# Optimization experiments

Hardware: AMD Instinct MI355X
Metric: run time of the kernel (lower is better)

The kernel has to match this reference:

```python
import jax, jax.numpy as jnp
import numpy as np

STRIDES = (4, 8, 16, 32, 64)
RATIOS = (0.5, 1.0, 2.0)
SCALE = 8.0
A = 3
PRE_NMS = 2000
MAX_PER_IMG = 1000
NMS_THR = 0.7
MAX_RATIO = float(abs(np.log(16.0 / 1000.0)))  # wh_ratio_clip = 16/1000
LEVEL_OFFSET = 4096.0  # > max image coordinate, separates levels for batched NMS
FEAT_HW = ((208, 336), (104, 168), (52, 84), (26, 42), (13, 21))
N = 8


def grid_anchors(stride, H, W):
    # mmdet-style base anchors: scale 8, ratios (0.5,1,2), centered at 0
    r = jnp.asarray(RATIOS, jnp.float32)
    h_r = jnp.sqrt(r)
    w_r = 1.0 / h_r
    ws = stride * w_r * SCALE
    hs = stride * h_r * SCALE
    base = jnp.stack([-ws / 2, -hs / 2, ws / 2, hs / 2], axis=-1)  # [A,4]
    sx = jnp.arange(W, dtype=jnp.float32) * stride
    sy = jnp.arange(H, dtype=jnp.float32) * stride
    yy, xx = jnp.meshgrid(sy, sx, indexing='ij')
    shifts = jnp.stack([xx, yy, xx, yy], axis=-1).reshape(-1, 4)  # [H*W,4], row-major
    return (shifts[:, None, :] + base[None, :, :]).reshape(-1, 4)  # [H*W*A,4]


def decode(anchors, deltas, h, w):
    # DeltaXYWH decode with means 0, stds 1, clip to image
    px = (anchors[..., 0] + anchors[..., 2]) * 0.5
    py = (anchors[..., 1] + anchors[..., 3]) * 0.5
    pw = anchors[..., 2] - anchors[..., 0]
    ph = anchors[..., 3] - anchors[..., 1]
    dx, dy = deltas[..., 0], deltas[..., 1]
    dw = jnp.clip(deltas[..., 2], -MAX_RATIO, MAX_RATIO)
    dh = jnp.clip(deltas[..., 3], -MAX_RATIO, MAX_RATIO)
    gx = px + pw * dx
    gy = py + ph * dy
    gw = pw * jnp.exp(dw)
    gh = ph * jnp.exp(dh)
    x1 = jnp.clip(gx - gw * 0.5, 0.0, w)
    y1 = jnp.clip(gy - gh * 0.5, 0.0, h)
    x2 = jnp.clip(gx + gw * 0.5, 0.0, w)
    y2 = jnp.clip(gy + gh * 0.5, 0.0, h)
    return jnp.stack([x1, y1, x2, y2], axis=-1)


def iou_matrix(b):
    area = (b[:, 2] - b[:, 0]) * (b[:, 3] - b[:, 1])
    lt = jnp.maximum(b[:, None, :2], b[None, :, :2])
    rb = jnp.minimum(b[:, None, 2:], b[None, :, 2:])
    wh = jnp.clip(rb - lt, 0.0, None)
    inter = wh[..., 0] * wh[..., 1]
    union = area[:, None] + area[None, :] - inter
    return inter / jnp.maximum(union, 1e-6)


def _forward(cls_list, reg_list, image_h, image_w):
    scores_all, deltas_all, anchors_all, levels_all = [], [], [], []
    for lvl, (cls, reg) in enumerate(zip(cls_list, reg_list)):
        n, _, H, W = cls.shape
        anchors = grid_anchors(STRIDES[lvl], H, W)  # [H*W*A,4]
        s = jax.nn.sigmoid(jnp.transpose(cls, (0, 2, 3, 1)).reshape(n, -1))
        d = jnp.transpose(reg, (0, 2, 3, 1)).reshape(n, -1, 4)
        k = min(PRE_NMS, s.shape[1])  # topk pre-selection per level
        sv, si = jax.lax.top_k(s, k)
        dv = jnp.take_along_axis(d, si[..., None], axis=1)
        av = anchors[si]
        scores_all.append(sv)
        deltas_all.append(dv)
        anchors_all.append(av)
        levels_all.append(jnp.full((k,), lvl, jnp.int32))
    scores = jnp.concatenate(scores_all, axis=1)    # [N,M]
    deltas = jnp.concatenate(deltas_all, axis=1)    # [N,M,4]
    anchors = jnp.concatenate(anchors_all, axis=1)  # [N,M,4]
    levels = jnp.concatenate(levels_all)            # [M] (same per image)
    boxes = decode(anchors, deltas, float(image_h), float(image_w))
    # filter_boxes with min_area = prod((0,0)) = 0: keep boxes with area >= 0
    area = (boxes[..., 2] - boxes[..., 0]) * (boxes[..., 3] - boxes[..., 1])
    scores = jnp.where(area >= 0.0, scores, -1.0)
    M = boxes.shape[1]
    idxs = jnp.arange(M)

    def nms_one(bs):
        b_i, s_i = bs
        order = jnp.argsort(-s_i)
        b = b_i[order]
        s = s_i[order]
        lv = levels[order]
        # batched NMS: offset each level so cross-level boxes never overlap
        ob = jax.lax.stop_gradient(b + (lv.astype(b.dtype) * LEVEL_OFFSET)[:, None])
        iou = iou_matrix(ob)  # [M,M]

        def body(i, keep):
            sup = (iou[i] > NMS_THR) & (idxs > i) & keep[i]
            return keep & (~sup)

        keep = jax.lax.fori_loop(0, M, body, jnp.ones((M,), bool))
        rank = jnp.cumsum(keep.astype(jnp.int32)) - 1
        tgt = jnp.where(keep & (rank < MAX_PER_IMG), rank, MAX_PER_IMG)  # dump slot
        out_b = jnp.zeros((MAX_PER_IMG + 1, 4), b.dtype).at[tgt].set(b)[:MAX_PER_IMG]
        out_s = jnp.zeros((MAX_PER_IMG + 1,), s.dtype).at[tgt].set(s)[:MAX_PER_IMG]
        return out_b, out_s

    pb, ps = jax.lax.map(nms_one, (boxes, scores))  # sequential per image
    return pb, ps  # [N,1000,4], [N,1000] (zero-padded)


def setup_inputs() -> dict:
    key = jax.random.key(0)
    inp = {}
    for lvl, (H, W) in enumerate(FEAT_HW):
        k1 = jax.random.fold_in(key, 2 * lvl)
        k2 = jax.random.fold_in(key, 2 * lvl + 1)
        inp[f"class_out_{lvl}"] = jax.random.normal(k1, (N, A, H, W), jnp.float32)
        inp[f"reg_out_{lvl}"] = jax.random.normal(k2, (N, 4 * A, H, W), jnp.float32)
    inp["image_h"] = 832
    inp["image_w"] = 1344
    return inp


def reference(class_out_0, class_out_1, class_out_2, class_out_3, class_out_4,
              reg_out_0, reg_out_1, reg_out_2, reg_out_3, reg_out_4,
              image_h, image_w):
    cls_list = [class_out_0, class_out_1, class_out_2, class_out_3, class_out_4]
    reg_list = [reg_out_0, reg_out_1, reg_out_2, reg_out_3, reg_out_4]
    return _forward(cls_list, reg_list, image_h, image_w)
```

## Files before the change

kernel.cpp:

```cpp
#include <hip/hip_runtime.h>
#include <cmath>

#pragma clang fp contract(off)

namespace {
constexpr int NIMG = 8;
constexpr int NLVL = 5;
constexpr int LH[5]   = {208,104,52,26,13};
constexpr int LW[5]   = {336,168,84,42,21};
constexpr int LSTR[5] = {4,8,16,32,64};
constexpr int HWA[5]  = {209664,52416,13104,3276,819};
constexpr int KSEL[5] = {2000,2000,2000,2000,819};
constexpr int SOFF[5] = {0,2000,4000,6000,8000};
constexpr int MTOT    = 8819;
constexpr int CAP     = 6144;
constexpr int NPAIR   = NIMG*NLVL;
constexpr int CCUM[5] = {52,65,69,70,71};
constexpr int BLK_PER_IMG = 71;
constexpr int MASK_W  = 32;
constexpr int OUTK    = 1000;

constexpr size_t OFF_HIST   = 0;
constexpr size_t OFF_PKC    = 0;
constexpr size_t OFF_CNT    = 655360;
constexpr size_t OFF_THR    = 655520;
constexpr size_t ZERO_BYTES = 655680;
constexpr size_t OFF_CAND   = 655872;
constexpr size_t OFF_SELIDX = 1638912;
constexpr size_t OFF_SELKEY = 1921120;
constexpr size_t OFF_SELSC  = 2485536;
constexpr size_t OFF_SELBOX = 2767744;
constexpr size_t OFF_MASK   = 3896576;
constexpr size_t OFF_CKEY   = OFF_MASK;
constexpr size_t OFF_KEEP   = 24376576;
}

struct Ins {
  const float* cls[5];
  const float* reg[5];
  const int* ih;
  const int* iw;
};

__device__ __forceinline__ void decode_block(int b, int& img, int& lvl, int& chunk) {
  img = b / BLK_PER_IMG;
  int rb = b - img*BLK_PER_IMG;
  if      (rb < CCUM[0]) { lvl=0; chunk=rb; }
  else if (rb < CCUM[1]) { lvl=1; chunk=rb-CCUM[0]; }
  else if (rb < CCUM[2]) { lvl=2; chunk=rb-CCUM[1]; }
  else if (rb < CCUM[3]) { lvl=3; chunk=rb-CCUM[2]; }
  else                   { lvl=4; chunk=0; }
}

__device__ __forceinline__ unsigned mapbits(float x) {
  unsigned u = __float_as_uint(x);
  return u ^ (unsigned)(((int)u >> 31) | (int)0x80000000);
}

__device__ __forceinline__ float sigmoid_ref(float x) {
  float e = (float)exp(-(double)x);
  return 1.0f / (1.0f + e);
}

__global__ void k_hist(Ins in, unsigned* __restrict__ hist) {
  int img, lvl, chunk; decode_block(blockIdx.x, img, lvl, chunk);
  __shared__ unsigned lh[4096];
  for (int i = threadIdx.x; i < 4096; i += 256) lh[i] = 0;
  __syncthreads();
  const float* src = in.cls[lvl] + (size_t)img * HWA[lvl];
  int base = chunk * 4096;
  #pragma unroll
  for (int j = 0; j < 16; j++) {
    int e = base + j*256 + threadIdx.x;
    if (e < HWA[lvl]) {
      unsigned m = mapbits(src[e]);
      atomicAdd(&lh[m >> 20], 1u);
    }
  }
  __syncthreads();
  unsigned* gh = hist + (img*NLVL + lvl) * 4096;
  for (int i = threadIdx.x; i < 4096; i += 256)
    if (lh[i]) atomicAdd(&gh[i], lh[i]);
}

__global__ void k_scan(const unsigned* __restrict__ hist, unsigned* __restrict__ thr) {
  int pair = blockIdx.x; int lvl = pair % NLVL;
  const unsigned* h = hist + (size_t)pair * 4096;
  __shared__ unsigned part[256];
  unsigned s = 0;
  #pragma unroll
  for (int i = 0; i < 16; i++) s += h[threadIdx.x*16 + i];
  part[threadIdx.x] = s;
  __syncthreads();
  if (threadIdx.x == 0) {
    unsigned k = (unsigned)KSEL[lvl];
    unsigned cum = 0;
    unsigned edge = 0;
    for (int t = 255; t >= 0; t--) {
      if (cum + part[t] >= k) {
        for (int b = t*16 + 15; b >= t*16; b--) {
          cum += h[b];
          if (cum >= k) { edge = (unsigned)b; break; }
        }
        thr[pair] = edge << 20;
        return;
      }
      cum += part[t];
    }
    thr[pair] = 0u;
  }
}

__global__ void __launch_bounds__(256) k_compact(Ins in, const unsigned* __restrict__ thr,
                          unsigned* __restrict__ cnt, unsigned* __restrict__ cand,
                          unsigned long long* __restrict__ ckey) {
  int img, lvl, chunk; decode_block(blockIdx.x, img, lvl, chunk);
  int pair = img*NLVL + lvl;
  unsigned T = thr[pair];
  const float* src = in.cls[lvl] + (size_t)img * HWA[lvl];
  int hw = LH[lvl] * LW[lvl];
  int base = chunk * 4096;
  int lid = threadIdx.x & 63;
  __shared__ unsigned lbuf[4096];
  __shared__ unsigned long long lkey[4096];
  __shared__ unsigned lc, gbase;
  if (threadIdx.x == 0) lc = 0;
  __syncthreads();
  #pragma unroll
  for (int j = 0; j < 16; j++) {
    int e = base + j*256 + threadIdx.x;
    float v = 0.0f;
    bool inb = (e < HWA[lvl]);
    if (inb) v = src[e];
    bool sel = inb && (mapbits(v) >= T);
    unsigned long long mask = __ballot(sel);
    if (mask != 0ull) {
      int leader = __ffsll((long long)mask) - 1;
      unsigned wb = 0;
      if (lid == leader) wb = atomicAdd(&lc, (unsigned)__popcll(mask));
      wb = (unsigned)__shfl((int)wb, leader, 64);
      if (sel) {
        unsigned p = wb + (unsigned)__popcll(mask & ((1ull << lid) - 1ull));
        int a = e / hw;
        int r = e - a*hw;
        unsigned idx = (unsigned)(r*3 + a);
        lbuf[p] = idx;
        float s = sigmoid_ref(v);
        unsigned pack = ((unsigned)lvl << 18) | idx;
        lkey[p] = ((unsigned long long)__float_as_uint(s) << 21)
                | (unsigned long long)(0x1FFFFFu - pack);
      }
    }
  }
  __syncthreads();
  if (threadIdx.x == 0) gbase = atomicAdd(&cnt[pair], lc);
  __syncthreads();
  unsigned nsel = lc, gb = gbase;
  for (unsigned t = threadIdx.x; t < nsel; t += 256) {
    unsigned p = gb + t;
    if (p < CAP) {
      cand[(size_t)pair*CAP + p] = lbuf[t];
      ckey[(size_t)pair*CAP + p] = lkey[t];
    }
  }
}

__global__ void __launch_bounds__(256) k_rank(const unsigned* __restrict__ cntA,
                       const unsigned* __restrict__ cand,
                       const unsigned long long* __restrict__ ckey,
                       unsigned* __restrict__ sel_idx,
                       unsigned long long* __restrict__ sel_key,
                       float* __restrict__ sel_sc) {
  int pair = blockIdx.y; int tile = blockIdx.x;
  int img = pair / NLVL, lvl = pair % NLVL;
  int c = min((int)cntA[pair], CAP);
  if (tile*256 >= c) return;
  __shared__ unsigned long long keys[CAP];
  const unsigned long long* kp = ckey + (size_t)pair*CAP;
  for (int j = threadIdx.x; j < c; j += 256) keys[j] = kp[j];
  __syncthreads();
  int jj = tile*256 + threadIdx.x;
  if (jj >= c) return;
  unsigned long long mykey = keys[jj];
  int rk = 0;
  for (int j = 0; j < c; j++) rk += (keys[j] > mykey) ? 1 : 0;
  if (rk < KSEL[lvl]) {
    int slot = img*MTOT + SOFF[lvl] + rk;
    sel_idx[slot] = cand[(size_t)pair*CAP + jj];
    sel_key[slot] = mykey;
    sel_sc[slot]  = __uint_as_float((unsigned)(mykey >> 21));
  }
}

__global__ void k_decode(Ins in, const unsigned* __restrict__ sel_idx,
                         float* __restrict__ sel_box) {
  int t = blockIdx.x*256 + threadIdx.x;
  if (t >= NIMG*MTOT) return;
  int img = t / MTOT, pos = t - img*MTOT;
  int lvl = pos<2000?0 : pos<4000?1 : pos<6000?2 : pos<8000?3 : 4;
  unsigned idx = sel_idx[img*MTOT + pos];
  int a = (int)(idx % 3u);
  int r = (int)(idx / 3u);
  int Wl = LW[lvl]; int hw = LH[lvl]*Wl;
  int x = r % Wl, y = r / Wl;
  const float* rg = in.reg[lvl] + (size_t)img * 4 * HWA[lvl];
  float dx = rg[(a*4+0)*hw + r];
  float dy = rg[(a*4+1)*hw + r];
  float dw = rg[(a*4+2)*hw + r];
  float dh = rg[(a*4+3)*hw + r];
  float ratio = (a==0) ? 0.5f : (a==1) ? 1.0f : 2.0f;
  float hr = sqrtf(ratio);
  float wr = 1.0f / hr;
  float st = (float)LSTR[lvl];
  float wsz = st * wr * 8.0f;
  float hsz = st * hr * 8.0f;
  float xs = (float)x * st, ys = (float)y * st;
  float x1 = xs - wsz*0.5f, x2 = xs + wsz*0.5f;
  float y1 = ys - hsz*0.5f, y2 = ys + hsz*0.5f;
  float px = (x1 + x2) * 0.5f, py = (y1 + y2) * 0.5f;
  float pw = x2 - x1,          ph = y2 - y1;
  const float MR = 4.135166556742356f;
  dw = fminf(fmaxf(dw, -MR), MR);
  dh = fminf(fmaxf(dh, -MR), MR);
  float gx = px + pw*dx, gy = py + ph*dy;
  float gw = pw * (float)exp((double)dw);
  float gh = ph * (float)exp((double)dh);
  float Wi = (float)(*in.iw), Hi = (float)(*in.ih);
  float4 bb;
  bb.x = fminf(fmaxf(gx - gw*0.5f, 0.0f), Wi);
  bb.y = fminf(fmaxf(gy - gh*0.5f, 0.0f), Hi);
  bb.z = fminf(fmaxf(gx + gw*0.5f, 0.0f), Wi);
  bb.w = fminf(fmaxf(gy + gh*0.5f, 0.0f), Hi);
  ((float4*)sel_box)[img*MTOT + pos] = bb;
}

__global__ void __launch_bounds__(256) k_masks(const float* __restrict__ sel_box,
                        unsigned long long* __restrict__ maskbuf) {
  int pair = blockIdx.y; int lvl = pair % NLVL; int img = pair / NLVL;
  int n = KSEL[lvl];
  int nw = (n + 63) >> 6;
  int wv = threadIdx.x >> 6;
  int lane = threadIdx.x & 63;
  int t = blockIdx.x * 4 + wv;
  int ntile = nw * (nw + 1) / 2;
  if (t >= ntile) return;
  int rb = 0, cum = 0;
  while (cum + (nw - rb) <= t) { cum += nw - rb; rb++; }
  int jw = rb + (t - cum);
  const float4* boxes = ((const float4*)sel_box) + img*MTOT + SOFF[lvl];
  float off = (float)lvl * 4096.0f;
  int col = jw*64 + lane;
  float bjx, bjy, bjz, bjw2, aj;
  if (col < n) {
    float4 bj = boxes[col];
    bjx = bj.x + off; bjy = bj.y + off; bjz = bj.z + off; bjw2 = bj.w + off;
    aj = (bjz - bjx) * (bjw2 - bjy);
  } else {
    bjx = 3.0e8f; bjy = 3.0e8f; bjz = 3.0e8f; bjw2 = 3.0e8f;
    aj = 0.0f;
  }
  __shared__ float4 srow[4][64];
  int row0 = rb*64;
  {
    float4 bi0 = boxes[min(row0 + lane, n-1)];
    bi0.x += off; bi0.y += off; bi0.z += off; bi0.w += off;
    srow[wv][lane] = bi0;
  }
  const double Md = 0.70000001788139343261718750;
  unsigned long long acc = 0ull;
  if (jw > rb) {
    #pragma unroll 16
    for (int r = 0; r < 64; r++) {
      float4 bi = srow[wv][r];
      float ai = (bi.z - bi.x) * (bi.w - bi.y);
      float xx1 = fmaxf(bi.x, bjx), yy1 = fmaxf(bi.y, bjy);
      float xx2 = fminf(bi.z, bjz), yy2 = fminf(bi.w, bjw2);
      float iw_ = fmaxf(xx2 - xx1, 0.0f), ih_ = fmaxf(yy2 - yy1, 0.0f);
      float inter = iw_ * ih_;
      float u = fmaxf((ai + aj) - inter, 1e-6f);
      bool sup = (double)inter >= Md * (double)u;
      unsigned long long word = __ballot(sup);
      if (lane == r) acc = word;
    }
  } else {
    #pragma unroll 16
    for (int r = 0; r < 64; r++) {
      float4 bi = srow[wv][r];
      float ai = (bi.z - bi.x) * (bi.w - bi.y);
      float xx1 = fmaxf(bi.x, bjx), yy1 = fmaxf(bi.y, bjy);
      float xx2 = fminf(bi.z, bjz), yy2 = fminf(bi.w, bjw2);
      float iw_ = fmaxf(xx2 - xx1, 0.0f), ih_ = fmaxf(yy2 - yy1, 0.0f);
      float inter = iw_ * ih_;
      float u = fmaxf((ai + aj) - inter, 1e-6f);
      bool sup = (double)inter >= Md * (double)u;
      unsigned long long word = __ballot(sup) & ~((2ull << r) - 1ull);
      if (lane == r) acc = word;
    }
  }
  if (row0 + lane < n)
    maskbuf[(size_t)pair*2000*MASK_W + (size_t)(row0 + lane)*MASK_W + jw] = acc;
}

__global__ void __launch_bounds__(1024) k_nms(const unsigned long long* __restrict__ maskbuf,
                      unsigned long long* __restrict__ keep) {
  int pair = blockIdx.x; int lvl = pair % NLVL;
  int n = KSEL[lvl];
  int nw = (n + 63) >> 6;
  const unsigned long long* mrow = maskbuf + (size_t)pair*2000*MASK_W;
  int tid = threadIdx.x;
  int w  = tid & 31;
  int rg = tid >> 5;
  __shared__ unsigned long long rem[32];
  __shared__ unsigned long long diag[64];
  __shared__ unsigned long long sSk;
  if (tid < 32) rem[tid] = 0ull;
  __syncthreads();

  unsigned long long A0, A1, B0, B1;
  {
    int r0 = min(rg*2, n-1), r1 = min(rg*2+1, n-1);
    A0 = mrow[(size_t)r0*MASK_W + w];
    A1 = mrow[(size_t)r1*MASK_W + w];
  }
  for (int k = 0; k < nw; k++) {
    if (k + 1 < nw) {
      int r0 = min(64*(k+1) + rg*2, n-1), r1 = min(64*(k+1) + rg*2 + 1, n-1);
      B0 = mrow[(size_t)r0*MASK_W + w];
      B1 = mrow[(size_t)r1*MASK_W + w];
    }
    if (w == k) { diag[rg*2] = A0; diag[rg*2+1] = A1; }
    __syncthreads();
    if (tid < 64) {
      int row = 64*k + tid;
      bool valid = row < n;
      unsigned long long D = valid ? diag[tid] : 0ull;
      unsigned long long rk = rem[k];
      unsigned long long S = rk;
      for (int it = 0; it < 64; it++) {
        bool kept = valid && !((S >> tid) & 1ull);
        unsigned long long c = kept ? D : 0ull;
        #pragma unroll
        for (int m = 1; m < 64; m <<= 1) {
          unsigned lo = (unsigned)__shfl_xor((int)(unsigned)(c & 0xffffffffull), m, 64);
          unsigned hi = (unsigned)__shfl_xor((int)(unsigned)(c >> 32), m, 64);
          c |= ((unsigned long long)hi << 32) | (unsigned long long)lo;
        }
        unsigned long long Snew = rk | c;
        if (Snew == S) break;
        S = Snew;
      }
      if (tid == 0) {
        sSk = S;
        int nb = n - 64*k;
        unsigned long long vm = (nb >= 64) ? ~0ull : ((1ull << nb) - 1ull);
        keep[(size_t)pair*MASK_W + k] = (~S) & vm;
      }
    }
    __syncthreads();
    if (w > k) {
      unsigned long long Sk = sSk;
      int r0 = 64*k + rg*2, r1 = r0 + 1;
      unsigned long long m = 0ull;
      if (r0 < n && !((Sk >> (rg*2)) & 1ull))     m |= A0;
      if (r1 < n && !((Sk >> (rg*2+1)) & 1ull))   m |= A1;
      if (m) atomicOr(&rem[w], m);
    }
    __syncthreads();
    A0 = B0; A1 = B1;
  }
}

__global__ void __launch_bounds__(64) k_pfx(const unsigned long long* __restrict__ keep,
                                            int* __restrict__ pkc) {
  int pair = blockIdx.x; int lvl = pair % NLVL;
  int n = KSEL[lvl];
  int nw = (n + 63) >> 6;
  int lane = threadIdx.x;
  unsigned long long w = (lane < nw) ? keep[(size_t)pair*MASK_W + lane] : 0ull;
  if (lane == nw - 1 && (n & 63)) w &= (1ull << (n & 63)) - 1ull;
  __shared__ int lcnt[64];
  lcnt[lane] = __popcll(w);
  __syncthreads();
  int pre = 0;
  for (int t = 0; t < lane; t++) pre += lcnt[t];
  for (int b = 0; b < 64; b++) {
    int p = lane*64 + b;
    if (p < n) {
      pre += (int)((w >> b) & 1ull);
      pkc[pair*2048 + p] = pre;
    }
  }
}

__global__ void __launch_bounds__(256) k_out2(const unsigned long long* __restrict__ sel_key,
                      const float* __restrict__ sel_box,
                      const unsigned long long* __restrict__ keep,
                      const int* __restrict__ pkc,
                      float* __restrict__ out) {
  int img = blockIdx.y;
  int pos = blockIdx.x*256 + threadIdx.x;
  if (pos >= MTOT) return;
  int lvl = pos<2000?0 : pos<4000?1 : pos<6000?2 : pos<8000?3 : 4;
  int local = pos - SOFF[lvl];
  int pair = img*NLVL + lvl;
  unsigned long long kw = keep[(size_t)pair*MASK_W + (local >> 6)];
  if (!((kw >> (local & 63)) & 1ull)) return;
  unsigned long long mykey = sel_key[img*MTOT + pos];
  int rank = pkc[pair*2048 + local] - 1;
  #pragma unroll
  for (int l2 = 0; l2 < NLVL; l2++) {
    if (l2 == lvl) continue;
    const unsigned long long* A = sel_key + img*MTOT + SOFF[l2];
    int lo = 0, hi = KSEL[l2];
    while (lo < hi) {
      int mid = (lo + hi) >> 1;
      if (A[mid] > mykey) lo = mid + 1; else hi = mid;
    }
    if (lo > 0) rank += pkc[(img*NLVL + l2)*2048 + lo - 1];
  }
  if (rank < OUTK) {
    ((float4*)out)[img*OUTK + rank] = ((const float4*)sel_box)[img*MTOT + pos];
    out[NIMG*OUTK*4 + img*OUTK + rank] = __uint_as_float((unsigned)(mykey >> 21));
  }
}

extern "C" void kernel_launch(void* const* d_in, const int* in_sizes, int n_in,
                              void* d_out, int out_size, void* d_ws, size_t ws_size,
                              hipStream_t stream) {
  Ins in;
  for (int l = 0; l < 5; l++) {
    in.cls[l] = (const float*)d_in[2*l];
    in.reg[l] = (const float*)d_in[2*l + 1];
  }
  in.ih = (const int*)d_in[10];
  in.iw = (const int*)d_in[11];

  char* ws = (char*)d_ws;
  unsigned* hist              = (unsigned*)(ws + OFF_HIST);
  int* pkc                    = (int*)(ws + OFF_PKC);
  unsigned* cnt               = (unsigned*)(ws + OFF_CNT);
  unsigned* thr               = (unsigned*)(ws + OFF_THR);
  unsigned* cand              = (unsigned*)(ws + OFF_CAND);
  unsigned* sel_idx           = (unsigned*)(ws + OFF_SELIDX);
  unsigned long long* sel_key = (unsigned long long*)(ws + OFF_SELKEY);
  float* sel_sc               = (float*)(ws + OFF_SELSC);
  float* sel_box              = (float*)(ws + OFF_SELBOX);
  unsigned long long* maskbuf = (unsigned long long*)(ws + OFF_MASK);
  unsigned long long* ckey    = (unsigned long long*)(ws + OFF_CKEY);
  unsigned long long* keep    = (unsigned long long*)(ws + OFF_KEEP);
  float* out                  = (float*)d_out;

  hipMemsetAsync(d_ws, 0, ZERO_BYTES, stream);
  hipMemsetAsync(d_out, 0, (size_t)NIMG*OUTK*5*sizeof(float), stream);

  k_hist   <<<NIMG*BLK_PER_IMG, 256, 0, stream>>>(in, hist);
  k_scan   <<<NPAIR, 256, 0, stream>>>(hist, thr);
  k_compact<<<NIMG*BLK_PER_IMG, 256, 0, stream>>>(in, thr, cnt, cand, ckey);
  k_rank   <<<dim3(CAP/256, NPAIR), 256, 0, stream>>>(cnt, cand, ckey, sel_idx, sel_key, sel_sc);
  k_decode <<<(NIMG*MTOT + 255)/256, 256, 0, stream>>>(in, sel_idx, sel_box);
  k_masks  <<<dim3(132, NPAIR), 256, 0, stream>>>(sel_box, maskbuf);
  k_nms    <<<NPAIR, 1024, 0, stream>>>(maskbuf, keep);
  k_pfx    <<<NPAIR, 64, 0, stream>>>(keep, pkc);
  k_out2   <<<dim3((MTOT + 255)/256, NIMG), 256, 0, stream>>>(sel_key, sel_box, keep, pkc, out);
}
```

Measured before the change: 283.5 us.

## Fuse decode into rank, prefix into NMS, vectorize score loads

Box decoding moves into the rank kernel, which now writes boxes straight to the selected slot, so the separate decode launch and the sel_idx buffer go away. The keep-count prefix computation moves into the tail of the NMS kernel, using shared keep words, which removes the k_pfx launch. The histogram and compaction kernels read class scores as float4 for levels 0-3, with a scalar path kept for level 4. Together this cuts two kernel launches and some global traffic, at the cost of more work and branch divergence inside k_rank.

```diff
diff --git a/kernel.cpp b/kernel.cpp
--- a/kernel.cpp
+++ b/kernel.cpp
@@ -68,13 +68,27 @@
   for (int i = threadIdx.x; i < 4096; i += 256) lh[i] = 0;
   __syncthreads();
   const float* src = in.cls[lvl] + (size_t)img * HWA[lvl];
-  int base = chunk * 4096;
-  #pragma unroll
-  for (int j = 0; j < 16; j++) {
-    int e = base + j*256 + threadIdx.x;
-    if (e < HWA[lvl]) {
-      unsigned m = mapbits(src[e]);
-      atomicAdd(&lh[m >> 20], 1u);
+  if (lvl != 4) {
+    const float4* src4 = (const float4*)src;
+    int nf4 = HWA[lvl] >> 2;
+    int base4 = chunk * 1024;
+    #pragma unroll
+    for (int j = 0; j < 4; j++) {
+      int f = base4 + j*256 + threadIdx.x;
+      if (f < nf4) {
+        float4 v = src4[f];
+        atomicAdd(&lh[mapbits(v.x) >> 20], 1u);
+        atomicAdd(&lh[mapbits(v.y) >> 20], 1u);
+        atomicAdd(&lh[mapbits(v.z) >> 20], 1u);
+        atomicAdd(&lh[mapbits(v.w) >> 20], 1u);
+      }
+    }
+  } else {
+    int base = chunk * 4096;
+    #pragma unroll
+    for (int j = 0; j < 16; j++) {
+      int e = base + j*256 + threadIdx.x;
+      if (e < HWA[4]) atomicAdd(&lh[mapbits(src[e]) >> 20], 1u);
     }
   }
   __syncthreads();
@@ -119,20 +133,14 @@
   unsigned T = thr[pair];
   const float* src = in.cls[lvl] + (size_t)img * HWA[lvl];
   int hw = LH[lvl] * LW[lvl];
-  int base = chunk * 4096;
   int lid = threadIdx.x & 63;
   __shared__ unsigned lbuf[4096];
   __shared__ unsigned long long lkey[4096];
   __shared__ unsigned lc, gbase;
   if (threadIdx.x == 0) lc = 0;
   __syncthreads();
-  #pragma unroll
-  for (int j = 0; j < 16; j++) {
-    int e = base + j*256 + threadIdx.x;
-    float v = 0.0f;
-    bool inb = (e < HWA[lvl]);
-    if (inb) v = src[e];
-    bool sel = inb && (mapbits(v) >= T);
+
+  auto emit = [&](int e, float v, bool sel) {
     unsigned long long mask = __ballot(sel);
     if (mask != 0ull) {
       int leader = __ffsll((long long)mask) - 1;
@@ -151,6 +159,34 @@
                 | (unsigned long long)(0x1FFFFFu - pack);
       }
     }
+  };
+
+  if (lvl != 4) {
+    const float4* src4 = (const float4*)src;
+    int nf4 = HWA[lvl] >> 2;
+    int base4 = chunk * 1024;
+    #pragma unroll
+    for (int j = 0; j < 4; j++) {
+      int f = base4 + j*256 + threadIdx.x;
+      bool inb = f < nf4;
+      float4 v4 = make_float4(0.f, 0.f, 0.f, 0.f);
+      if (inb) v4 = src4[f];
+      int e0 = f * 4;
+      emit(e0+0, v4.x, inb && (mapbits(v4.x) >= T));
+      emit(e0+1, v4.y, inb && (mapbits(v4.y) >= T));
+      emit(e0+2, v4.z, inb && (mapbits(v4.z) >= T));
+      emit(e0+3, v4.w, inb && (mapbits(v4.w) >= T));
+    }
+  } else {
+    int base = chunk * 4096;
+    #pragma unroll
+    for (int j = 0; j < 16; j++) {
+      int e = base + j*256 + threadIdx.x;
+      float v = 0.0f;
+      bool inb = (e < HWA[4]);
+      if (inb) v = src[e];
+      emit(e, v, inb && (mapbits(v) >= T));
+    }
   }
   __syncthreads();
   if (threadIdx.x == 0) gbase = atomicAdd(&cnt[pair], lc);
@@ -165,12 +201,12 @@
   }
 }
 
-__global__ void __launch_bounds__(256) k_rank(const unsigned* __restrict__ cntA,
+__global__ void __launch_bounds__(256) k_rank(Ins in, const unsigned* __restrict__ cntA,
                        const unsigned* __restrict__ cand,
                        const unsigned long long* __restrict__ ckey,
-                       unsigned* __restrict__ sel_idx,
                        unsigned long long* __restrict__ sel_key,
-                       float* __restrict__ sel_sc) {
+                       float* __restrict__ sel_sc,
+                       float* __restrict__ sel_box) {
   int pair = blockIdx.y; int tile = blockIdx.x;
   int img = pair / NLVL, lvl = pair % NLVL;
   int c = min((int)cntA[pair], CAP);
@@ -186,52 +222,43 @@
   for (int j = 0; j < c; j++) rk += (keys[j] > mykey) ? 1 : 0;
   if (rk < KSEL[lvl]) {
     int slot = img*MTOT + SOFF[lvl] + rk;
-    sel_idx[slot] = cand[(size_t)pair*CAP + jj];
     sel_key[slot] = mykey;
     sel_sc[slot]  = __uint_as_float((unsigned)(mykey >> 21));
-  }
-}
-
-__global__ void k_decode(Ins in, const unsigned* __restrict__ sel_idx,
-                         float* __restrict__ sel_box) {
-  int t = blockIdx.x*256 + threadIdx.x;
-  if (t >= NIMG*MTOT) return;
-  int img = t / MTOT, pos = t - img*MTOT;
-  int lvl = pos<2000?0 : pos<4000?1 : pos<6000?2 : pos<8000?3 : 4;
-  unsigned idx = sel_idx[img*MTOT + pos];
-  int a = (int)(idx % 3u);
-  int r = (int)(idx / 3u);
-  int Wl = LW[lvl]; int hw = LH[lvl]*Wl;
-  int x = r % Wl, y = r / Wl;
-  const float* rg = in.reg[lvl] + (size_t)img * 4 * HWA[lvl];
-  float dx = rg[(a*4+0)*hw + r];
-  float dy = rg[(a*4+1)*hw + r];
-  float dw = rg[(a*4+2)*hw + r];
-  float dh = rg[(a*4+3)*hw + r];
-  float ratio = (a==0) ? 0.5f : (a==1) ? 1.0f : 2.0f;
-  float hr = sqrtf(ratio);
-  float wr = 1.0f / hr;
-  float st = (float)LSTR[lvl];
-  float wsz = st * wr * 8.0f;
-  float hsz = st * hr * 8.0f;
-  float xs = (float)x * st, ys = (float)y * st;
-  float x1 = xs - wsz*0.5f, x2 = xs + wsz*0.5f;
-  float y1 = ys - hsz*0.5f, y2 = ys + hsz*0.5f;
-  float px = (x1 + x2) * 0.5f, py = (y1 + y2) * 0.5f;
-  float pw = x2 - x1,          ph = y2 - y1;
-  const float MR = 4.135166556742356f;
-  dw = fminf(fmaxf(dw, -MR), MR);
-  dh = fminf(fmaxf(dh, -MR), MR);
-  float gx = px + pw*dx, gy = py + ph*dy;
-  float gw = pw * (float)exp((double)dw);
-  float gh = ph * (float)exp((double)dh);
-  float Wi = (float)(*in.iw), Hi = (float)(*in.ih);
-  float4 bb;
-  bb.x = fminf(fmaxf(gx - gw*0.5f, 0.0f), Wi);
-  bb.y = fminf(fmaxf(gy - gh*0.5f, 0.0f), Hi);
-  bb.z = fminf(fmaxf(gx + gw*0.5f, 0.0f), Wi);
-  bb.w = fminf(fmaxf(gy + gh*0.5f, 0.0f), Hi);
-  ((float4*)sel_box)[img*MTOT + pos] = bb;
+    unsigned idx = cand[(size_t)pair*CAP + jj];
+    int a = (int)(idx % 3u);
+    int r = (int)(idx / 3u);
+    int Wl = LW[lvl]; int hw = LH[lvl]*Wl;
+    int x = r % Wl, y = r / Wl;
+    const float* rg = in.reg[lvl] + (size_t)img * 4 * HWA[lvl];
+    float dx = rg[(a*4+0)*hw + r];
+    float dy = rg[(a*4+1)*hw + r];
+    float dw = rg[(a*4+2)*hw + r];
+    float dh = rg[(a*4+3)*hw + r];
+    float ratio = (a==0) ? 0.5f : (a==1) ? 1.0f : 2.0f;
+    float hr = sqrtf(ratio);
+    float wr = 1.0f / hr;
+    float st = (float)LSTR[lvl];
+    float wsz = st * wr * 8.0f;
+    float hsz = st * hr * 8.0f;
+    float xs = (float)x * st, ys = (float)y * st;
+    float x1 = xs - wsz*0.5f, x2 = xs + wsz*0.5f;
+    float y1 = ys - hsz*0.5f, y2 = ys + hsz*0.5f;
+    float px = (x1 + x2) * 0.5f, py = (y1 + y2) * 0.5f;
+    float pw = x2 - x1,          ph = y2 - y1;
+    const float MR = 4.135166556742356f;
+    dw = fminf(fmaxf(dw, -MR), MR);
+    dh = fminf(fmaxf(dh, -MR), MR);
+    float gx = px + pw*dx, gy = py + ph*dy;
+    float gw = pw * (float)exp((double)dw);
+    float gh = ph * (float)exp((double)dh);
+    float Wi = (float)(*in.iw), Hi = (float)(*in.ih);
+    float4 bb;
+    bb.x = fminf(fmaxf(gx - gw*0.5f, 0.0f), Wi);
+    bb.y = fminf(fmaxf(gy - gh*0.5f, 0.0f), Hi);
+    bb.z = fminf(fmaxf(gx + gw*0.5f, 0.0f), Wi);
+    bb.w = fminf(fmaxf(gy + gh*0.5f, 0.0f), Hi);
+    ((float4*)sel_box)[slot] = bb;
+  }
 }
 
 __global__ void __launch_bounds__(256) k_masks(const float* __restrict__ sel_box,
@@ -302,7 +329,7 @@
 }
 
 __global__ void __launch_bounds__(1024) k_nms(const unsigned long long* __restrict__ maskbuf,
-                      unsigned long long* __restrict__ keep) {
+                      unsigned long long* __restrict__ keep, int* __restrict__ pkc) {
   int pair = blockIdx.x; int lvl = pair % NLVL;
   int n = KSEL[lvl];
   int nw = (n + 63) >> 6;
@@ -312,8 +339,10 @@
   int rg = tid >> 5;
   __shared__ unsigned long long rem[32];
   __shared__ unsigned long long diag[64];
+  __shared__ unsigned long long skw[32];
   __shared__ unsigned long long sSk;
-  if (tid < 32) rem[tid] = 0ull;
+  __shared__ int lcnt[64];
+  if (tid < 32) { rem[tid] = 0ull; skw[tid] = 0ull; }
   __syncthreads();
 
   unsigned long long A0, A1, B0, B1;
@@ -353,7 +382,9 @@
         sSk = S;
         int nb = n - 64*k;
         unsigned long long vm = (nb >= 64) ? ~0ull : ((1ull << nb) - 1ull);
-        keep[(size_t)pair*MASK_W + k] = (~S) & vm;
+        unsigned long long kw = (~S) & vm;
+        skw[k] = kw;
+        keep[(size_t)pair*MASK_W + k] = kw;
       }
     }
     __syncthreads();
@@ -368,26 +399,18 @@
     __syncthreads();
     A0 = B0; A1 = B1;
   }
-}
-
-__global__ void __launch_bounds__(64) k_pfx(const unsigned long long* __restrict__ keep,
-                                            int* __restrict__ pkc) {
-  int pair = blockIdx.x; int lvl = pair % NLVL;
-  int n = KSEL[lvl];
-  int nw = (n + 63) >> 6;
-  int lane = threadIdx.x;
-  unsigned long long w = (lane < nw) ? keep[(size_t)pair*MASK_W + lane] : 0ull;
-  if (lane == nw - 1 && (n & 63)) w &= (1ull << (n & 63)) - 1ull;
-  __shared__ int lcnt[64];
-  lcnt[lane] = __popcll(w);
-  __syncthreads();
-  int pre = 0;
-  for (int t = 0; t < lane; t++) pre += lcnt[t];
-  for (int b = 0; b < 64; b++) {
-    int p = lane*64 + b;
-    if (p < n) {
-      pre += (int)((w >> b) & 1ull);
-      pkc[pair*2048 + p] = pre;
+  if (tid < 64) {
+    int lane = tid;
+    unsigned long long kw = (lane < nw) ? skw[lane] : 0ull;
+    lcnt[lane] = __popcll(kw);
+    int pre = 0;
+    for (int t2 = 0; t2 < lane; t2++) pre += lcnt[t2];
+    for (int b = 0; b < 64; b++) {
+      int p = lane*64 + b;
+      if (p < n) {
+        pre += (int)((kw >> b) & 1ull);
+        pkc[pair*2048 + p] = pre;
+      }
     }
   }
 }
@@ -441,7 +464,6 @@
   unsigned* cnt               = (unsigned*)(ws + OFF_CNT);
   unsigned* thr               = (unsigned*)(ws + OFF_THR);
   unsigned* cand              = (unsigned*)(ws + OFF_CAND);
-  unsigned* sel_idx           = (unsigned*)(ws + OFF_SELIDX);
   unsigned long long* sel_key = (unsigned long long*)(ws + OFF_SELKEY);
   float* sel_sc               = (float*)(ws + OFF_SELSC);
   float* sel_box              = (float*)(ws + OFF_SELBOX);
@@ -456,10 +478,8 @@
   k_hist   <<<NIMG*BLK_PER_IMG, 256, 0, stream>>>(in, hist);
   k_scan   <<<NPAIR, 256, 0, stream>>>(hist, thr);
   k_compact<<<NIMG*BLK_PER_IMG, 256, 0, stream>>>(in, thr, cnt, cand, ckey);
-  k_rank   <<<dim3(CAP/256, NPAIR), 256, 0, stream>>>(cnt, cand, ckey, sel_idx, sel_key, sel_sc);
-  k_decode <<<(NIMG*MTOT + 255)/256, 256, 0, stream>>>(in, sel_idx, sel_box);
+  k_rank   <<<dim3(CAP/256, NPAIR), 256, 0, stream>>>(in, cnt, cand, ckey, sel_key, sel_sc, sel_box);
   k_masks  <<<dim3(132, NPAIR), 256, 0, stream>>>(sel_box, maskbuf);
-  k_nms    <<<NPAIR, 1024, 0, stream>>>(maskbuf, keep);
-  k_pfx    <<<NPAIR, 64, 0, stream>>>(keep, pkc);
+  k_nms    <<<NPAIR, 1024, 0, stream>>>(maskbuf, keep, pkc);
   k_out2   <<<dim3((MTOT + 255)/256, NIMG), 256, 0, stream>>>(sel_key, sel_box, keep, pkc, out);
 }
```

Result: faster. 277.5 us (-2.1%).
